# Performance work log

Hardware: AMD Instinct MI355X
Metric: run time of the kernel (lower is better)

The kernel has to match this reference:

```python
import jax, jax.numpy as jnp
import numpy as np

N_EMBID = 384
N_HEADS = 6
HEAD_SIZE = N_EMBID // N_HEADS
BLOCK_SIZE = 256
EPS = 1e-5


def _layernorm(x, g, b):
    mu = jnp.mean(x, axis=-1, keepdims=True)
    var = jnp.var(x, axis=-1, keepdims=True)
    return (x - mu) * jax.lax.rsqrt(var + EPS) * g + b


def setup_inputs() -> dict:
    key = jax.random.key(0)
    ks = jax.random.split(key, 12)
    B, T, C, H, D = 128, 256, N_EMBID, N_HEADS, HEAD_SIZE
    s_in = 1.0 / np.sqrt(C)
    s_hid = 1.0 / np.sqrt(4 * C)
    return {
        "x": jax.random.normal(ks[0], (B, T, C), dtype=jnp.float32),
        # per-head QKV projections stacked: [H, C, D] (jax convention y = x @ W)
        "wq": jax.random.normal(ks[1], (H, C, D), dtype=jnp.float32) * s_in,
        "wk": jax.random.normal(ks[2], (H, C, D), dtype=jnp.float32) * s_in,
        "wv": jax.random.normal(ks[3], (H, C, D), dtype=jnp.float32) * s_in,
        "w_proj": jax.random.normal(ks[4], (C, C), dtype=jnp.float32) * s_in,
        "b_proj": jnp.zeros((C,), dtype=jnp.float32),
        "w1": jax.random.normal(ks[5], (C, 4 * C), dtype=jnp.float32) * s_in,
        "b1": jnp.zeros((4 * C,), dtype=jnp.float32),
        "w2": jax.random.normal(ks[6], (4 * C, C), dtype=jnp.float32) * s_hid,
        "b2": jnp.zeros((C,), dtype=jnp.float32),
        "ln1_g": jnp.ones((C,), dtype=jnp.float32),
        "ln1_b": jnp.zeros((C,), dtype=jnp.float32),
        "ln2_g": jnp.ones((C,), dtype=jnp.float32),
        "ln2_b": jnp.zeros((C,), dtype=jnp.float32),
    }


def reference(x, wq, wk, wv, w_proj, b_proj, w1, b1, w2, b2,
              ln1_g, ln1_b, ln2_g, ln2_b):
    B, T, C = x.shape
    h = _layernorm(x, ln1_g, ln1_b)
    q = jnp.einsum('btc,hcd->bhtd', h, wq)
    k = jnp.einsum('btc,hcd->bhtd', h, wk)
    v = jnp.einsum('btc,hcd->bhtd', h, wv)
    # NOTE: original scales by C**-0.5 with C = full n_embid, not head_size
    scores = jnp.einsum('bhtd,bhsd->bhts', q, k) * (C ** -0.5)
    causal = jnp.tril(jnp.ones((T, T), dtype=bool))
    scores = jnp.where(causal, scores, -jnp.inf)
    wei = jax.nn.softmax(scores, axis=-1)  # dropout = identity (eval)
    attn = jnp.einsum('bhts,bhsd->bhtd', wei, v)
    attn = attn.transpose(0, 2, 1, 3).reshape(B, T, C)  # concat heads
    x = x + attn @ w_proj + b_proj
    h2 = _layernorm(x, ln2_g, ln2_b)
    mlp = jax.nn.relu(h2 @ w1 + b1) @ w2 + b2
    return x + mlp
```

## Files before the change

kernel.cpp:

```cpp
#include <hip/hip_runtime.h>
#include <stdint.h>

typedef unsigned short u16;
typedef unsigned int u32;
typedef __bf16 bf16x8_t __attribute__((ext_vector_type(8)));
typedef float f32x4_t __attribute__((ext_vector_type(4)));
typedef unsigned int u32x2 __attribute__((ext_vector_type(2)));
typedef unsigned int u32x4 __attribute__((ext_vector_type(4)));

union FragAB { bf16x8_t v; u32x2 q[2]; };
union Stage16 { u32x4 v; u16 e[8]; };

#define DEVFN static __device__ __forceinline__

DEVFN u16 f2bf(float f) {
    u32 x = __builtin_bit_cast(u32, f);
    return (u16)((x + 0x7fffu + ((x >> 16) & 1u)) >> 16);
}

DEVFN f32x4_t zero4() { f32x4_t z = {0.f, 0.f, 0.f, 0.f}; return z; }

#define SCALE_QK 0.051031036307982884f
#define NEG_BIG  -30000.0f

__global__ __launch_bounds__(256) void ln_kernel(
        const float* __restrict__ in, const float* __restrict__ g,
        const float* __restrict__ b, u16* __restrict__ out)
{
    const int lane = threadIdx.x & 63;
    const int w = threadIdx.x >> 6;
    const int row = blockIdx.x * 4 + w;
    const float* rp = in + (size_t)row * 384;
    float v[6];
    float s = 0.f, sq = 0.f;
    #pragma unroll
    for (int j = 0; j < 6; j++) {
        v[j] = rp[lane + j * 64];
        s += v[j];
        sq += v[j] * v[j];
    }
    #pragma unroll
    for (int o = 32; o >= 1; o >>= 1) {
        s  += __shfl_xor(s, o);
        sq += __shfl_xor(sq, o);
    }
    const float mean = s * (1.f / 384.f);
    const float var = sq * (1.f / 384.f) - mean * mean;
    const float rs = rsqrtf(var + 1e-5f);
    u16* op = out + (size_t)row * 384;
    #pragma unroll
    for (int j = 0; j < 6; j++) {
        const int c = lane + j * 64;
        op[c] = f2bf((v[j] - mean) * rs * g[c] + b[c]);
    }
}

__global__ void qkv_w_kernel(const float* __restrict__ wq, const float* __restrict__ wk,
                             const float* __restrict__ wv, u16* __restrict__ bt)
{
    const int idx = blockIdx.x * 256 + threadIdx.x;
    if (idx >= 1152 * 384) return;
    const int j = idx / 384, c = idx % 384;
    const int which = j / 384;
    const int r = j % 384;
    const int h = r / 64, d = r % 64;
    const float* w = (which == 0) ? wq : (which == 1 ? wk : wv);
    bt[idx] = f2bf(w[(h * 384 + c) * 64 + d]);
}

__global__ void transpose_w_kernel(const float* __restrict__ w, u16* __restrict__ bt,
                                   int K, int N)
{
    const int idx = blockIdx.x * 256 + threadIdx.x;
    if (idx >= K * N) return;
    const int n = idx / K, k = idx % K;
    bt[idx] = f2bf(w[(size_t)k * N + n]);
}

template<bool HAS_BIAS, bool HAS_RES, bool RELU, bool OUT_BF16>
__global__ __launch_bounds__(256) void gemm_kernel(
        const u16* __restrict__ A, const u16* __restrict__ Bt,
        const float* __restrict__ bias, const float* __restrict__ res,
        void* __restrict__ Out, int M, int N, int K)
{
    __shared__ u16 As[128 * 72];
    __shared__ u16 Bs[128 * 72];
    const int tid = threadIdx.x;
    const int lane = tid & 63;
    const int w = tid >> 6;
    const int tileN = blockIdx.x * 128;
    const int tileM = blockIdx.y * 128;
    (void)M;

    f32x4_t acc[4][4];
    #pragma unroll
    for (int i = 0; i < 4; i++)
        #pragma unroll
        for (int j = 0; j < 4; j++)
            acc[i][j] = zero4();

    const int m = lane & 15;
    const int g4 = (lane >> 4) * 4;
    const int srow = tid >> 3;
    const int scol = (tid & 7) * 8;

    for (int k0 = 0; k0 < K; k0 += 64) {
        #pragma unroll
        for (int i = 0; i < 4; i++) {
            const int r = i * 32 + srow;
            u32x4 av = *(const u32x4*)(A  + (size_t)(tileM + r) * K + k0 + scol);
            u32x4 bv = *(const u32x4*)(Bt + (size_t)(tileN + r) * K + k0 + scol);
            *(u32x4*)(&As[r * 72 + scol]) = av;
            *(u32x4*)(&Bs[r * 72 + scol]) = bv;
        }
        __syncthreads();

        FragAB af[4][2], bfb[4][2];
        #pragma unroll
        for (int mi = 0; mi < 4; mi++) {
            const u16* rp = &As[((w >> 1) * 64 + mi * 16 + m) * 72];
            #pragma unroll
            for (int ks = 0; ks < 2; ks++) {
                af[mi][ks].q[0] = *(const u32x2*)(rp + ks * 32 + g4);
                af[mi][ks].q[1] = *(const u32x2*)(rp + ks * 32 + 16 + g4);
            }
        }
        #pragma unroll
        for (int ni = 0; ni < 4; ni++) {
            const u16* rp = &Bs[((w & 1) * 64 + ni * 16 + m) * 72];
            #pragma unroll
            for (int ks = 0; ks < 2; ks++) {
                bfb[ni][ks].q[0] = *(const u32x2*)(rp + ks * 32 + g4);
                bfb[ni][ks].q[1] = *(const u32x2*)(rp + ks * 32 + 16 + g4);
            }
        }
        #pragma unroll
        for (int ks = 0; ks < 2; ks++)
            #pragma unroll
            for (int mi = 0; mi < 4; mi++)
                #pragma unroll
                for (int ni = 0; ni < 4; ni++)
                    acc[mi][ni] = __builtin_amdgcn_mfma_f32_16x16x32_bf16(
                        af[mi][ks].v, bfb[ni][ks].v, acc[mi][ni], 0, 0, 0);
        __syncthreads();
    }

    #pragma unroll
    for (int mi = 0; mi < 4; mi++) {
        #pragma unroll
        for (int ni = 0; ni < 4; ni++) {
            #pragma unroll
            for (int r = 0; r < 4; r++) {
                const int grow = tileM + (w >> 1) * 64 + mi * 16 + (lane >> 4) * 4 + r;
                const int gcol = tileN + (w & 1) * 64 + ni * 16 + (lane & 15);
                float v = acc[mi][ni][r];
                if (HAS_BIAS) v += bias[gcol];
                if (HAS_RES) v += res[(size_t)grow * N + gcol];
                if (RELU) v = fmaxf(v, 0.f);
                const size_t o = (size_t)grow * N + gcol;
                if (OUT_BF16) ((u16*)Out)[o] = f2bf(v);
                else ((float*)Out)[o] = v;
            }
        }
    }
}

__global__ __launch_bounds__(256) void attn_kernel(
        const u16* __restrict__ qkv, u16* __restrict__ out, int row0)
{
    __shared__ u16 Kl[256 * 72];
    __shared__ u16 Vt[64 * 264];
    __shared__ u16 Pl[4 * 16 * 264];

    const int bi = blockIdx.x / 6, h = blockIdx.x % 6;
    const int tid = threadIdx.x, lane = tid & 63, w = tid >> 6;
    const u16* base = qkv + (size_t)bi * 256 * 1152 + h * 64;

    #pragma unroll
    for (int pass = 0; pass < 8; pass++) {
        const int s = pass * 32 + (tid >> 3);
        const int d8 = (tid & 7) * 8;
        const u16* krow = base + (size_t)s * 1152;
        *(u32x4*)(&Kl[s * 72 + d8]) = *(const u32x4*)(krow + 384 + d8);
        Stage16 vv;
        vv.v = *(const u32x4*)(krow + 768 + d8);
        #pragma unroll
        for (int j = 0; j < 8; j++) Vt[(d8 + j) * 264 + s] = vv.e[j];
    }
    __syncthreads();

    const int m = lane & 15;
    const int g4 = (lane >> 4) * 4;
    u16* pw = &Pl[w * 16 * 264];

    for (int p = 0; p < 4; p++) {
        const int rt = p * 4 + w;
        const int rp = rt * 16;
        const int nt = rt + 1;

        FragAB qa[2];
        const u16* qrow = base + (size_t)(rp + m) * 1152;
        #pragma unroll
        for (int ks = 0; ks < 2; ks++) {
            qa[ks].q[0] = *(const u32x2*)(qrow + ks * 32 + g4);
            qa[ks].q[1] = *(const u32x2*)(qrow + ks * 32 + 16 + g4);
        }

        f32x4_t sacc[16];
        #pragma unroll
        for (int ct = 0; ct < 16; ct++) {
            if (ct < nt) {
                sacc[ct] = zero4();
                #pragma unroll
                for (int ks = 0; ks < 2; ks++) {
                    FragAB kb;
                    const u16* kr = &Kl[(ct * 16 + m) * 72 + ks * 32 + g4];
                    kb.q[0] = *(const u32x2*)(kr);
                    kb.q[1] = *(const u32x2*)(kr + 16);
                    sacc[ct] = __builtin_amdgcn_mfma_f32_16x16x32_bf16(
                        qa[ks].v, kb.v, sacc[ct], 0, 0, 0);
                }
            }
        }

        const int rbase = rp + (lane >> 4) * 4;
        float mx[4] = {-1e30f, -1e30f, -1e30f, -1e30f};
        #pragma unroll
        for (int ct = 0; ct < 16; ct++) if (ct < nt) {
            #pragma unroll
            for (int r = 0; r < 4; r++) {
                float v = sacc[ct][r] * SCALE_QK;
                if (ct * 16 + m > rbase + r) v = NEG_BIG;
                sacc[ct][r] = v;
                mx[r] = fmaxf(mx[r], v);
            }
        }
        #pragma unroll
        for (int r = 0; r < 4; r++) {
            #pragma unroll
            for (int o = 1; o < 16; o <<= 1) mx[r] = fmaxf(mx[r], __shfl_xor(mx[r], o));
        }
        float sum[4] = {0.f, 0.f, 0.f, 0.f};
        #pragma unroll
        for (int ct = 0; ct < 16; ct++) if (ct < nt) {
            #pragma unroll
            for (int r = 0; r < 4; r++) {
                const float e = __expf(sacc[ct][r] - mx[r]);
                sacc[ct][r] = e;
                sum[r] += e;
            }
        }
        #pragma unroll
        for (int r = 0; r < 4; r++) {
            #pragma unroll
            for (int o = 1; o < 16; o <<= 1) sum[r] += __shfl_xor(sum[r], o);
        }
        float inv[4];
        #pragma unroll
        for (int r = 0; r < 4; r++) inv[r] = 1.f / sum[r];

        #pragma unroll
        for (int ct = 0; ct < 16; ct++) if (ct < nt) {
            #pragma unroll
            for (int r = 0; r < 4; r++)
                pw[((lane >> 4) * 4 + r) * 264 + ct * 16 + m] = f2bf(sacc[ct][r] * inv[r]);
        }
        if (nt & 1) {
            #pragma unroll
            for (int r = 0; r < 4; r++)
                pw[((lane >> 4) * 4 + r) * 264 + nt * 16 + m] = 0;
        }

        const int kpairs = (nt + 1) >> 1;
        f32x4_t oacc[4];
        #pragma unroll
        for (int ni = 0; ni < 4; ni++) oacc[ni] = zero4();
        #pragma unroll
        for (int kk = 0; kk < 8; kk++) if (kk < kpairs) {
            FragAB pa;
            const u16* pr = &pw[m * 264 + kk * 32 + g4];
            pa.q[0] = *(const u32x2*)(pr);
            pa.q[1] = *(const u32x2*)(pr + 16);
            #pragma unroll
            for (int ni = 0; ni < 4; ni++) {
                FragAB vb;
                const u16* vr = &Vt[(ni * 16 + m) * 264 + kk * 32 + g4];
                vb.q[0] = *(const u32x2*)(vr);
                vb.q[1] = *(const u32x2*)(vr + 16);
                oacc[ni] = __builtin_amdgcn_mfma_f32_16x16x32_bf16(
                    pa.v, vb.v, oacc[ni], 0, 0, 0);
            }
        }

        #pragma unroll
        for (int ni = 0; ni < 4; ni++) {
            #pragma unroll
            for (int r = 0; r < 4; r++) {
                const int t = rp + (lane >> 4) * 4 + r;
                out[((size_t)row0 + bi * 256 + t) * 384 + h * 64 + ni * 16 + m] =
                    f2bf(oacc[ni][r]);
            }
        }
    }
}

extern "C" void kernel_launch(void* const* d_in, const int* in_sizes, int n_in,
                              void* d_out, int out_size, void* d_ws, size_t ws_size,
                              hipStream_t stream)
{
    (void)in_sizes; (void)n_in; (void)out_size;
    const float* x     = (const float*)d_in[0];
    const float* wq    = (const float*)d_in[1];
    const float* wk    = (const float*)d_in[2];
    const float* wv    = (const float*)d_in[3];
    const float* wproj = (const float*)d_in[4];
    const float* bproj = (const float*)d_in[5];
    const float* w1    = (const float*)d_in[6];
    const float* b1    = (const float*)d_in[7];
    const float* w2    = (const float*)d_in[8];
    const float* b2    = (const float*)d_in[9];
    const float* ln1g  = (const float*)d_in[10];
    const float* ln1b  = (const float*)d_in[11];
    const float* ln2g  = (const float*)d_in[12];
    const float* ln2b  = (const float*)d_in[13];
    float* out = (float*)d_out;

    char* ws = (char*)d_ws;
    u16* hattn  = (u16*)(ws);
    u16* wqkvT  = (u16*)(ws + 25165824);
    u16* wprojT = (u16*)(ws + 26050560);
    u16* w1T    = (u16*)(ws + 26345472);
    u16* w2T    = (u16*)(ws + 27525120);
    char* dyn   = ws + 28704768;
    const size_t avail = (ws_size > (size_t)28704768) ? ws_size - (size_t)28704768 : (size_t)0;

    int na = 32, nm = 32;
    for (int n = 1; n <= 32; n <<= 1) if ((size_t)75497472  / n <= avail) { na = n; break; }
    for (int n = 1; n <= 32; n <<= 1) if ((size_t)100663296 / n <= avail) { nm = n; break; }

    qkv_w_kernel<<<1728, 256, 0, stream>>>(wq, wk, wv, wqkvT);
    transpose_w_kernel<<<576, 256, 0, stream>>>(wproj, wprojT, 384, 384);
    transpose_w_kernel<<<2304, 256, 0, stream>>>(w1, w1T, 384, 1536);
    transpose_w_kernel<<<2304, 256, 0, stream>>>(w2, w2T, 1536, 384);

    ln_kernel<<<8192, 256, 0, stream>>>(x, ln1g, ln1b, hattn);

    const int rows_a = 32768 / na, bat_a = 128 / na;
    u16* qkvc = (u16*)dyn;
    for (int c = 0; c < na; c++) {
        const int row0 = c * rows_a;
        gemm_kernel<false, false, false, true><<<dim3(9, rows_a / 128), 256, 0, stream>>>(
            hattn + (size_t)row0 * 384, wqkvT, nullptr, nullptr, qkvc, rows_a, 1152, 384);
        attn_kernel<<<bat_a * 6, 256, 0, stream>>>(qkvc, hattn, row0);
    }

    gemm_kernel<true, true, false, false><<<dim3(3, 256), 256, 0, stream>>>(
        hattn, wprojT, bproj, x, out, 32768, 384, 384);

    ln_kernel<<<8192, 256, 0, stream>>>(out, ln2g, ln2b, hattn);

    const int rows_m = 32768 / nm;
    u16* mlp1c = (u16*)dyn;
    for (int c = 0; c < nm; c++) {
        const int row0 = c * rows_m;
        gemm_kernel<true, false, true, true><<<dim3(12, rows_m / 128), 256, 0, stream>>>(
            hattn + (size_t)row0 * 384, w1T, b1, nullptr, mlp1c, rows_m, 1536, 384);
        gemm_kernel<true, true, false, false><<<dim3(3, rows_m / 128), 256, 0, stream>>>(
            mlp1c, w2T, b2, out + (size_t)row0 * 384, out + (size_t)row0 * 384,
            rows_m, 384, 1536);
    }
}
```

Before: 473.1 us.

## Load GEMM tiles directly to LDS with XOR-swizzled layout

Replaces the register-staged global-to-shared tile copy in the GEMM kernel with global_load_lds direct-to-LDS 16-byte loads. The padded shared layout is replaced by an unpadded one that uses an XOR swizzle on 16-byte chunks to avoid bank conflicts on fragment reads. The aim is to cut VGPR traffic and LDS write instructions during staging. It depends on 16-byte global_load_lds support and correct swizzle indexing, and there is still no double buffering.

```diff
diff --git a/kernel.cpp b/kernel.cpp
--- a/kernel.cpp
+++ b/kernel.cpp
@@ -19,6 +19,12 @@
 }
 
 DEVFN f32x4_t zero4() { f32x4_t z = {0.f, 0.f, 0.f, 0.f}; return z; }
+
+typedef __attribute__((address_space(1))) void as1_void;
+typedef __attribute__((address_space(3))) void as3_void;
+
+#define GLOAD_LDS16(src, dst) \
+    __builtin_amdgcn_global_load_lds((as1_void*)(void*)(src), (as3_void*)(dst), 16, 0, 0)
 
 #define SCALE_QK 0.051031036307982884f
 #define NEG_BIG  -30000.0f
@@ -83,8 +89,8 @@
         const float* __restrict__ bias, const float* __restrict__ res,
         void* __restrict__ Out, int M, int N, int K)
 {
-    __shared__ u16 As[128 * 72];
-    __shared__ u16 Bs[128 * 72];
+    __shared__ u16 As[128 * 64];
+    __shared__ u16 Bs[128 * 64];
     const int tid = threadIdx.x;
     const int lane = tid & 63;
     const int w = tid >> 6;
@@ -100,38 +106,41 @@
             acc[i][j] = zero4();
 
     const int m = lane & 15;
-    const int g4 = (lane >> 4) * 4;
-    const int srow = tid >> 3;
-    const int scol = (tid & 7) * 8;
+    const int g8 = (lane >> 4) * 8;
 
     for (int k0 = 0; k0 < K; k0 += 64) {
         #pragma unroll
         for (int i = 0; i < 4; i++) {
-            const int r = i * 32 + srow;
-            u32x4 av = *(const u32x4*)(A  + (size_t)(tileM + r) * K + k0 + scol);
-            u32x4 bv = *(const u32x4*)(Bt + (size_t)(tileN + r) * K + k0 + scol);
-            *(u32x4*)(&As[r * 72 + scol]) = av;
-            *(u32x4*)(&Bs[r * 72 + scol]) = bv;
+            const int r = (w * 4 + i) * 8 + (lane >> 3);
+            const int sc = (lane & 7) ^ (r & 7);
+            GLOAD_LDS16(A + (size_t)(tileM + r) * K + k0 + sc * 8,
+                        (char*)As + (w * 4 + i) * 1024);
+            GLOAD_LDS16(Bt + (size_t)(tileN + r) * K + k0 + sc * 8,
+                        (char*)Bs + (w * 4 + i) * 1024);
         }
         __syncthreads();
 
         FragAB af[4][2], bfb[4][2];
         #pragma unroll
         for (int mi = 0; mi < 4; mi++) {
-            const u16* rp = &As[((w >> 1) * 64 + mi * 16 + m) * 72];
+            const int ar = (w >> 1) * 64 + mi * 16 + m;
+            const char* rp = (const char*)As + ar * 128;
+            const int sw = (ar & 7) << 4;
             #pragma unroll
             for (int ks = 0; ks < 2; ks++) {
-                af[mi][ks].q[0] = *(const u32x2*)(rp + ks * 32 + g4);
-                af[mi][ks].q[1] = *(const u32x2*)(rp + ks * 32 + 16 + g4);
+                af[mi][ks].q[0] = *(const u32x2*)(rp + ((ks * 64 + g8) ^ sw));
+                af[mi][ks].q[1] = *(const u32x2*)(rp + ((ks * 64 + 32 + g8) ^ sw));
             }
         }
         #pragma unroll
         for (int ni = 0; ni < 4; ni++) {
-            const u16* rp = &Bs[((w & 1) * 64 + ni * 16 + m) * 72];
+            const int br = (w & 1) * 64 + ni * 16 + m;
+            const char* rp = (const char*)Bs + br * 128;
+            const int sw = (br & 7) << 4;
             #pragma unroll
             for (int ks = 0; ks < 2; ks++) {
-                bfb[ni][ks].q[0] = *(const u32x2*)(rp + ks * 32 + g4);
-                bfb[ni][ks].q[1] = *(const u32x2*)(rp + ks * 32 + 16 + g4);
+                bfb[ni][ks].q[0] = *(const u32x2*)(rp + ((ks * 64 + g8) ^ sw));
+                bfb[ni][ks].q[1] = *(const u32x2*)(rp + ((ks * 64 + 32 + g8) ^ sw));
             }
         }
         #pragma unroll
```

New measurement: 458.6 us. 3.1% less time.
